# Optimization experiments

Hardware: AMD Instinct MI355X
Metric: run time of the kernel (lower is better)

Reference implementation:

```python
import jax, jax.numpy as jnp
import numpy as np

INPUT_SIZE = 500
SENTENCE_SIZE = 128


def setup_inputs() -> dict:
    key = jax.random.key(0)
    ks = jax.random.split(key, 20)
    B, D = 16, 512
    Ho, Hi, Hu = 4, 4, 4
    dh_ori = D // Ho          # 128
    dh = D // (Hi + Hu)       # 64
    s = 0.05
    code = jax.random.normal(ks[0], (B, INPUT_SIZE, D), jnp.float32)
    # binary sentence-membership mask (which code tokens belong to each sentence)
    input_sentence = (jax.random.uniform(ks[1], (B, SENTENCE_SIZE, INPUT_SIZE)) < 0.2).astype(jnp.float32)

    def W(k, h, dout):
        return jax.random.normal(k, (h, D, dout), jnp.float32) * s

    def b(k, h, dout):
        return jax.random.normal(k, (h, dout), jnp.float32) * 0.01

    return dict(
        code=code, input_sentence=input_sentence,
        Wq_ori=W(ks[2], Ho, dh_ori), bq_ori=b(ks[3], Ho, dh_ori),
        Wk_ori=W(ks[4], Ho, dh_ori), bk_ori=b(ks[5], Ho, dh_ori),
        Wq_in=W(ks[6], Hi, dh), bq_in=b(ks[7], Hi, dh),
        Wk_in=W(ks[8], Hi, dh), bk_in=b(ks[9], Hi, dh),
        Wv_in=W(ks[10], Hi, dh), bv_in=b(ks[11], Hi, dh),
        Wq_out=W(ks[12], Hu, dh), bq_out=b(ks[13], Hu, dh),
        Wk_out=W(ks[14], Hu, dh), bk_out=b(ks[15], Hu, dh),
        Wv_out=W(ks[16], Hu, dh), bv_out=b(ks[17], Hu, dh),
    )


def _proj(x, W, b):
    # x: (B, N, D), W: (H, D, F), b: (H, F) -> (B, H, N, F), relu Dense per head
    return jax.nn.relu(jnp.einsum('bnd,hdf->bhnf', x, W) + b[:, None, :])


def reference(code, input_sentence,
              Wq_ori, bq_ori, Wk_ori, bk_ori,
              Wq_in, bq_in, Wk_in, bk_in, Wv_in, bv_in,
              Wq_out, bq_out, Wk_out, bk_out, Wv_out, bv_out):
    B, S = input_sentence.shape[0], input_sentence.shape[1]
    sent = input_sentence

    # ---- original (ori) branch: max over heads of raw QK^T, mask, matmul code ----
    q = _proj(code, Wq_ori, bq_ori)
    k = _proj(code, Wk_ori, bk_ori)
    scores_ori = jnp.einsum('bhnf,bhmf->bhnm', q, k).max(axis=1)      # (B, N, N)
    sA = jnp.einsum('bsn,bnm->bsm', sent, scores_ori)                 # (B, S, N)
    out_ori = jnp.einsum('bsm,bmd->bsd', sent * sA, code)             # (B, S, D)

    # ---- in-mask heads ----
    qi = _proj(code, Wq_in, bq_in)
    ki = _proj(code, Wk_in, bk_in)
    vi = _proj(code, Wv_in, bv_in)
    sc = jnp.einsum('bhnf,bhmf->bhnm', qi, ki)                        # (B, Hi, N, N)
    sAi = jnp.einsum('bsn,bhnm->bhsm', sent, sc)                      # (B, Hi, S, N)
    out_in = jnp.einsum('bhsm,bhmf->bhsf', sent[:, None] * sAi, vi)   # (B, Hi, S, F)

    # ---- out-mask heads ----
    qo = _proj(code, Wq_out, bq_out)
    ko = _proj(code, Wk_out, bk_out)
    vo = _proj(code, Wv_out, bv_out)
    sco = jnp.einsum('bhnf,bhmf->bhnm', qo, ko)
    sAo = jnp.einsum('bsn,bhnm->bhsm', sent, sco)
    masked = (sent - 1.0)[:, None] * sAo                              # (B, Hu, S, N)
    include = sent.sum(axis=2)[:, None, :, None]                      # (B, 1, S, 1)
    masked = masked / (INPUT_SIZE - include) * include
    out_out = jnp.einsum('bhsm,bhmf->bhsf', masked, vo)               # (B, Hu, S, F)

    # original returns a list [ori, in_0..in_Hi-1, out_0..out_Hu-1]; concat along features
    in_flat = jnp.transpose(out_in, (0, 2, 1, 3)).reshape(B, S, -1)
    out_flat = jnp.transpose(out_out, (0, 2, 1, 3)).reshape(B, S, -1)
    return jnp.concatenate([out_ori, in_flat, out_flat], axis=-1)
```

## Files before the change

### kernel.cpp

```cpp
#include <hip/hip_runtime.h>
#include <cfloat>

#define B_  16
#define N_  500
#define NP  512
#define S_  128
#define D_  512
#define FO  128
#define FI  64

typedef unsigned short u16;
typedef __attribute__((ext_vector_type(8))) short bf8;
typedef __attribute__((ext_vector_type(4))) float f4;

#define MFMA(a,b,c) __builtin_amdgcn_mfma_f32_16x16x32_bf16((a),(b),(c),0,0,0)

__device__ __forceinline__ u16 f2b(float x){
    union{float f;unsigned u;} v; v.f=x;
    unsigned r = v.u + 0x7fffu + ((v.u>>16)&1u);
    return (u16)(r>>16);
}
__device__ __forceinline__ float b2f(u16 x){
    union{unsigned u;float f;} v; v.u=((unsigned)x)<<16; return v.f;
}
__device__ __forceinline__ bf8 ldb8(const u16* p){ return *(const bf8*)p; }

__device__ __forceinline__ void gl2lds16(const u16* g, u16* lds){
    __builtin_amdgcn_global_load_lds(
        (const __attribute__((address_space(1))) unsigned int*)g,
        (__attribute__((address_space(3))) unsigned int*)lds, 16, 0, 0);
}
__device__ __forceinline__ void vdrain(){
    asm volatile("s_waitcnt vmcnt(0)" ::: "memory");
}

struct PWAll { const float* W[8]; u16* WT[8]; };
__global__ __launch_bounds__(256) void prep_fused(const float* __restrict__ code,
                                                  u16* __restrict__ codeB,
                                                  u16* __restrict__ codeT,
                                                  PWAll a,
                                                  const float* __restrict__ sent,
                                                  u16* __restrict__ sentB,
                                                  float* __restrict__ inc,
                                                  u16* a0, u16* a1, u16* a2, u16* a3)
{
    __shared__ float T[64][65];
    const int t = threadIdx.x;
    const int x = blockIdx.x;
    if (x < 1024){
        const int b  = x >> 6;
        const int m0 = ((x >> 3) & 7) * 64;
        const int d0 = (x & 7) * 64;
        #pragma unroll
        for (int i=0;i<16;++i){
            int idx = t + i*256; int rr = idx>>6, cc = idx&63;
            int m = m0+rr;
            T[rr][cc] = (m < N_) ? code[((size_t)b*N_+m)*D_ + d0+cc] : 0.f;
        }
        __syncthreads();
        #pragma unroll
        for (int i=0;i<16;++i){
            int idx=t+i*256; int rr=idx>>6, cc=idx&63; int m=m0+rr;
            if (m<N_) codeB[((size_t)b*N_+m)*D_ + d0+cc] = f2b(T[rr][cc]);
        }
        #pragma unroll
        for (int i=0;i<16;++i){
            int idx=t+i*256; int dd=idx>>6, mm=idx&63;
            codeT[((size_t)b*D_ + d0+dd)*NP + m0+mm] = f2b(T[mm][dd]);
        }
    } else if (x < 1344){
        const int v    = x - 1024;
        const int h    = v / 80;
        const int rem  = v - h*80;
        const int slot = rem >> 3;
        const int d0   = (rem & 7) * 64;
        const int widx = slot<4 ? (slot>>1) : slot-2;
        const int ftile= slot<4 ? (slot&1)  : 0;
        const int F    = slot<4 ? 128 : 64;
        const float* W = a.W[widx];
        u16* WT        = a.WT[widx];
        const int f0 = ftile*64;
        #pragma unroll
        for (int i=0;i<16;++i){
            int idx=t+i*256; int rr=idx>>6, cc=idx&63;
            T[rr][cc] = W[((size_t)h*D_ + d0+rr)*F + f0+cc];
        }
        __syncthreads();
        #pragma unroll
        for (int i=0;i<16;++i){
            int idx=t+i*256; int ff=idx>>6, dd=idx&63;
            WT[((size_t)h*F + f0+ff)*D_ + d0+dd] = f2b(T[dd][ff]);
        }
    } else if (x < 2368){
        const int y  = x - 1344;
        const int b  = y >> 6;
        const int s  = (y & 63)*2 + (t >> 7);
        const int tl = t & 127;
        const float* row = sent + ((size_t)b*S_+s)*N_;
        float4 v = make_float4(0.f,0.f,0.f,0.f);
        const int n = tl*4;
        if (n < N_) v = *(const float4*)(row+n);
        float sum = v.x+v.y+v.z+v.w;
        ushort4 o; o.x=f2b(v.x); o.y=f2b(v.y); o.z=f2b(v.z); o.w=f2b(v.w);
        *(ushort4*)&sentB[((size_t)b*S_+s)*NP + n] = o;
        #pragma unroll
        for (int off=32; off; off>>=1) sum += __shfl_down(sum, off);
        __shared__ float ls[4];
        if ((t&63)==0) ls[t>>6]=sum;
        __syncthreads();
        if (tl==0) inc[b*S_+s] = ls[(t>>7)*2] + ls[(t>>7)*2+1];
    } else {
        const int u  = x - 2368;
        u16* arr4[4] = {a0,a1,a2,a3};
        u16* base = arr4[u>>6] + (size_t)(u&63)*FI*NP;
        for (int idx=t; idx<FI*12; idx+=256){
            int f = idx/12, n = N_ + idx%12;
            base[(size_t)f*NP + n] = 0;
        }
    }
}

struct GemmOut { const float* bias[8]; u16* dst[8]; };
union ProjLDS {
    u16 ab[4][4096];
    u16 ot[16896];
};
__global__ __launch_bounds__(256) void proj_gemm(const u16* __restrict__ codeB,
                                                 const u16* __restrict__ WallT,
                                                 GemmOut go)
{
    __shared__ alignas(16) ProjLDS L;

    const int t = threadIdx.x;
    const int w = t>>6, l = t&63, lane16 = l&15, lq = l>>4;
    const int bid = blockIdx.x;
    const int xcd = bid & 7;
    const int g   = bid >> 3;
    const int rt  = xcd*8 + g/20;
    const int ct  = g - (g/20)*20;
    const int r0 = rt*128;
    const int c0 = ct*128;
    const int wr = (w>>1)*64, wc = (w&1)*64;
    const int srow = l>>2;

    f4 acc[4][4] = {};

    auto STAGE = [&](u16* Ad, u16* Bd, int k0){
        #pragma unroll
        for (int iss=0; iss<2; ++iss){
            const int rbase = w*32 + iss*16;
            const int R  = rbase + srow;
            const int cg = ((l&3) ^ ((R>>1)&3))*8;
            gl2lds16(codeB + (size_t)(r0+R)*D_ + k0 + cg, Ad + rbase*32);
            gl2lds16(WallT + (size_t)(c0+R)*D_ + k0 + cg, Bd + rbase*32);
        }
    };
    auto COMPUTE = [&](const u16* Ad, const u16* Bd){
        bf8 af[4], bfr[4];
        #pragma unroll
        for (int i=0;i<4;++i){
            const int Ra = wr + i*16 + lane16;
            const int Rb = wc + i*16 + lane16;
            af[i]  = *(const bf8*)&Ad[Ra*32 + ((lq ^ ((Ra>>1)&3))*8)];
            bfr[i] = *(const bf8*)&Bd[Rb*32 + ((lq ^ ((Rb>>1)&3))*8)];
        }
        #pragma unroll
        for (int i=0;i<4;++i)
            #pragma unroll
            for (int j=0;j<4;++j)
                acc[i][j] = MFMA(af[i], bfr[j], acc[i][j]);
    };

    STAGE(L.ab[0], L.ab[2], 0);
    #pragma unroll
    for (int k0=0; k0<D_; k0+=64){
        vdrain(); __syncthreads();
        if (k0+32 < D_) STAGE(L.ab[1], L.ab[3], k0+32);
        COMPUTE(L.ab[0], L.ab[2]);
        vdrain(); __syncthreads();
        if (k0+64 < D_) STAGE(L.ab[0], L.ab[2], k0+64);
        COMPUTE(L.ab[1], L.ab[3]);
    }

    const int ri = (ct<4) ? 0 : (ct<8) ? 1 : 2 + ((ct-8)>>1);
    const bool tr = (ri==2)||(ri==4)||(ri==5)||(ri==7);

    vdrain(); __syncthreads();

    #pragma unroll
    for (int j=0;j<4;++j){
        const int c = c0 + wc + j*16 + lane16;
        const int idx = (c < 1024) ? (c & 511) : ((c-1024) & 255);
        const float bv = go.bias[ri][idx];
        if (tr){
            #pragma unroll
            for (int i=0;i<4;++i){
                ushort4 o4;
                float x0=acc[i][j][0]+bv, x1=acc[i][j][1]+bv, x2=acc[i][j][2]+bv, x3=acc[i][j][3]+bv;
                o4.x=f2b(x0>0.f?x0:0.f); o4.y=f2b(x1>0.f?x1:0.f);
                o4.z=f2b(x2>0.f?x2:0.f); o4.w=f2b(x3>0.f?x3:0.f);
                *(ushort4*)&L.ot[(wc+j*16+lane16)*132 + wr+i*16+lq*4] = o4;
            }
        } else {
            #pragma unroll
            for (int i=0;i<4;++i)
                #pragma unroll
                for (int reg=0;reg<4;++reg){
                    float x = acc[i][j][reg] + bv;
                    L.ot[(wr+i*16+lq*4+reg)*132 + wc+j*16+lane16] = f2b(x>0.f?x:0.f);
                }
        }
    }
    __syncthreads();

    if (tr){
        const int c  = t>>1;
        const int cg = c0 + c;
        const int u  = cg - 1024;
        const int hfv = u & 255, h = hfv>>6, f2 = hfv & 63;
        u16* dbase = go.dst[ri];
        const int half = t & 1;
        #pragma unroll
        for (int k2=0;k2<16;++k2){
            const int r  = half*64 + k2*4;
            const int rb = r0 + r;
            if (rb < 8000){
                const int b = rb/500, n = rb - b*500;
                *(ushort4*)&dbase[((size_t)(b*4+h)*FI + f2)*NP + n] =
                    *(const ushort4*)&L.ot[c*132 + r];
            }
        }
    } else {
        const int r  = t>>1;
        const int rb = r0 + r;
        if (rb < 8000){
            const int b = rb/500, n = rb - b*500;
            const int half = t & 1;
            const int cg0 = c0 + half*64;
            int h, f2base, F2;
            if (cg0 < 1024){ const int hf0 = cg0 & 511; h = hf0>>7; f2base = hf0 & 127; F2 = 128; }
            else           { const int hf0 = (cg0-1024) & 255; h = hf0>>6; f2base = hf0 & 63; F2 = 64; }
            u16* dstp = go.dst[ri] + ((size_t)(b*4+h)*N_ + n)*F2 + f2base;
            #pragma unroll
            for (int k2=0;k2<16;++k2)
                *(ushort4*)&dstp[k2*4] = *(const ushort4*)&L.ot[r*132 + half*64 + k2*4];
        }
    }
}

struct AttnArgs { const u16* qT[2]; const u16* kp[2]; const u16* vT[2]; };
struct MsLDS  { u16 Qs[64][136]; u16 Ks[128][136]; };
struct AtLDS  { float red[4][32][68]; u16 qsS[32][72]; u16 Pw[4][32][72]; };
union MALDS   { MsLDS ms; AtLDS at; };

__global__ __launch_bounds__(256) void msattn(const u16* __restrict__ q,
                                              const u16* __restrict__ k,
                                              u16* __restrict__ maxscT,
                                              AttnArgs a,
                                              const u16* __restrict__ sentB,
                                              const float* __restrict__ inc,
                                              float* __restrict__ out)
{
    __shared__ alignas(16) MALDS L;
    const int t=threadIdx.x, w=t>>6, l=t&63, lane16=l&15, lq=l>>4;
    const int idx = blockIdx.x >> 1;

    if ((blockIdx.x & 1) == 0){
        const int b=idx&15, n0=((idx>>4)&7)*64, m0=(idx>>7)*128;
        const int wr=(w>>1)*32, wc=(w&1)*64;

        f4 best[2][4];
        #pragma unroll
        for(int rt=0;rt<2;++rt)
            #pragma unroll
            for(int ct=0;ct<4;++ct)
                #pragma unroll
                for(int i=0;i<4;++i) best[rt][ct][i] = -FLT_MAX;

        for (int h=0;h<4;++h){
            const u16* qh = q + (size_t)(b*4+h)*N_*FO;
            const u16* kh = k + (size_t)(b*4+h)*N_*FO;
            #pragma unroll
            for (int i=0;i<4;++i){
                const int e=t+i*256, row=e>>4, kc=(e&15)*8;
                int n=n0+row; if(n>N_-1)n=N_-1;
                *(bf8*)&L.ms.Qs[row][kc] = ldb8(qh + (size_t)n*FO + kc);
            }
            #pragma unroll
            for (int i=0;i<8;++i){
                const int e=t+i*256, row=e>>4, kc=(e&15)*8;
                int m=m0+row; if(m>N_-1)m=N_-1;
                *(bf8*)&L.ms.Ks[row][kc] = ldb8(kh + (size_t)m*FO + kc);
            }
            __syncthreads();
            f4 acc[2][4]={};
            #pragma unroll
            for (int kk=0;kk<FO;kk+=32){
                bf8 a0=*(const bf8*)&L.ms.Qs[wr+lane16][kk+lq*8];
                bf8 a1=*(const bf8*)&L.ms.Qs[wr+16+lane16][kk+lq*8];
                #pragma unroll
                for(int ct=0;ct<4;++ct){
                    bf8 bb=*(const bf8*)&L.ms.Ks[wc+ct*16+lane16][kk+lq*8];
                    acc[0][ct]=MFMA(a0,bb,acc[0][ct]);
                    acc[1][ct]=MFMA(a1,bb,acc[1][ct]);
                }
            }
            #pragma unroll
            for(int rt=0;rt<2;++rt)
                #pragma unroll
                for(int ct=0;ct<4;++ct)
                    #pragma unroll
                    for(int i=0;i<4;++i) best[rt][ct][i] = fmaxf(best[rt][ct][i], acc[rt][ct][i]);
            __syncthreads();
        }
        #pragma unroll
        for(int rt=0;rt<2;++rt)
            #pragma unroll
            for(int ct=0;ct<4;++ct){
                const int m  = m0+wc+ct*16+lane16;
                const int nb = n0+wr+rt*16+lq*4;
                ushort4 o; o.x=f2b(best[rt][ct][0]); o.y=f2b(best[rt][ct][1]);
                o.z=f2b(best[rt][ct][2]); o.w=f2b(best[rt][ct][3]);
                *(ushort4*)&maxscT[((size_t)b*NP+m)*NP + nb] = o;
            }
    } else {
        const int bh=idx&63, b=bh>>2, h=bh&3, s0=((idx>>6)&3)*32, br=idx>>8;
        const u16* qT = a.qT[br];
        const u16* kp = a.kp[br];
        const u16* vT = a.vT[br];

        {
            const u16 *ap[2], *bp[4];
            #pragma unroll
            for(int rt=0;rt<2;++rt) ap[rt] = sentB + ((size_t)b*S_ + s0+rt*16+lane16)*NP + w*128 + lq*8;
            #pragma unroll
            for(int ct=0;ct<4;++ct) bp[ct] = qT + ((size_t)bh*FI + ct*16+lane16)*NP + w*128 + lq*8;
            f4 acc[2][4] = {};
            #pragma unroll
            for (int k0=0;k0<128;k0+=32){
                bf8 a0=ldb8(ap[0]+k0), a1=ldb8(ap[1]+k0);
                #pragma unroll
                for(int ct=0;ct<4;++ct){
                    bf8 bb=ldb8(bp[ct]+k0);
                    acc[0][ct]=MFMA(a0,bb,acc[0][ct]);
                    acc[1][ct]=MFMA(a1,bb,acc[1][ct]);
                }
            }
            #pragma unroll
            for(int rt=0;rt<2;++rt)
                #pragma unroll
                for(int ct=0;ct<4;++ct)
                    #pragma unroll
                    for(int reg=0;reg<4;++reg)
                        L.at.red[w][rt*16+lq*4+reg][ct*16+lane16] = acc[rt][ct][reg];
        }
        __syncthreads();
        {
            const int s=t>>3, f0=(t&7)*8;
            #pragma unroll
            for (int j=0;j<8;++j){
                float v = L.at.red[0][s][f0+j]+L.at.red[1][s][f0+j]
                        + L.at.red[2][s][f0+j]+L.at.red[3][s][f0+j];
                L.at.qsS[s][f0+j] = f2b(v);
            }
        }
        __syncthreads();

        f4 accO[2][4] = {};
        #pragma unroll
        for (int c=0;c<2;++c){
            const int m0 = w*64 + c*256;
            f4 p[2][4] = {};
            const u16* bp[4];
            #pragma unroll
            for(int ct=0;ct<4;++ct){
                int m=m0+ct*16+lane16; if(m>N_-1)m=N_-1;
                bp[ct] = kp + ((size_t)bh*N_+m)*FI + lq*8;
            }
            #pragma unroll
            for (int kk=0; kk<FI; kk+=32){
                bf8 a0 = *(const bf8*)&L.at.qsS[lane16][kk+lq*8];
                bf8 a1 = *(const bf8*)&L.at.qsS[16+lane16][kk+lq*8];
                #pragma unroll
                for(int ct=0;ct<4;++ct){
                    bf8 bb=ldb8(bp[ct]+kk);
                    p[0][ct]=MFMA(a0,bb,p[0][ct]);
                    p[1][ct]=MFMA(a1,bb,p[1][ct]);
                }
            }
            #pragma unroll
            for(int rt=0;rt<2;++rt)
                #pragma unroll
                for(int ct=0;ct<4;++ct){
                    const int m = m0+ct*16+lane16;
                    #pragma unroll
                    for(int reg=0;reg<4;++reg){
                        const int s = s0+rt*16+lq*4+reg;
                        const float sv = b2f(sentB[((size_t)b*S_+s)*NP+m]);
                        const float wgt = br ? ((m<N_)? sv-1.f : 0.f) : sv;
                        L.at.Pw[w][rt*16+lq*4+reg][ct*16+lane16] = f2b(p[rt][ct][reg]*wgt);
                    }
                }
            #pragma unroll
            for (int kk2=0; kk2<64; kk2+=32){
                bf8 a2[2];
                #pragma unroll
                for(int rt=0;rt<2;++rt) a2[rt] = *(const bf8*)&L.at.Pw[w][rt*16+lane16][kk2+lq*8];
                #pragma unroll
                for(int ct=0;ct<4;++ct){
                    bf8 vv = ldb8(vT + ((size_t)bh*FI + ct*16+lane16)*NP + m0+kk2+lq*8);
                    accO[0][ct]=MFMA(a2[0],vv,accO[0][ct]);
                    accO[1][ct]=MFMA(a2[1],vv,accO[1][ct]);
                }
            }
        }
        #pragma unroll
        for(int rt=0;rt<2;++rt)
            #pragma unroll
            for(int ct=0;ct<4;++ct)
                #pragma unroll
                for(int reg=0;reg<4;++reg)
                    L.at.red[w][rt*16+lq*4+reg][ct*16+lane16] = accO[rt][ct][reg];
        __syncthreads();
        {
            const int s=t>>3, f0=(t&7)*8;
            float fac = 1.f;
            if (br){ const float ic = inc[b*S_+s0+s]; fac = ic/(500.f-ic); }
            const size_t o = ((size_t)b*S_+s0+s)*1024 + (br?768:512) + h*FI + f0;
            #pragma unroll
            for (int j=0;j<8;++j){
                float v = L.at.red[0][s][f0+j]+L.at.red[1][s][f0+j]
                        + L.at.red[2][s][f0+j]+L.at.red[3][s][f0+j];
                out[o+j] = v*fac;
            }
        }
    }
}

__global__ __launch_bounds__(512) void saoo(const u16* __restrict__ sentB,
                                            const u16* __restrict__ maxscT,
                                            const u16* __restrict__ codeT,
                                            float* __restrict__ out)
{
    __shared__ u16 sAmS[16][520];
    const int b=blockIdx.x, s0=blockIdx.y*16;
    const int t=threadIdx.x, w=t>>6, l=t&63, lane16=l&15, lq=l>>4;

    {
        const int m0 = w*64;
        const u16* ap = sentB + ((size_t)b*S_ + s0+lane16)*NP + lq*8;
        const u16* bp[4];
        #pragma unroll
        for(int ct=0;ct<4;++ct) bp[ct] = maxscT + ((size_t)b*NP + m0+ct*16+lane16)*NP + lq*8;
        f4 acc[4] = {};
        for (int k0=0;k0<NP;k0+=32){
            bf8 av=ldb8(ap+k0);
            #pragma unroll
            for(int ct=0;ct<4;++ct) acc[ct]=MFMA(av, ldb8(bp[ct]+k0), acc[ct]);
        }
        #pragma unroll
        for(int ct=0;ct<4;++ct){
            const int m = m0+ct*16+lane16;
            #pragma unroll
            for(int reg=0;reg<4;++reg){
                const int s = s0+lq*4+reg;
                const float sv = b2f(sentB[((size_t)b*S_+s)*NP+m]);
                sAmS[lq*4+reg][m] = (sv != 0.f) ? f2b(acc[ct][reg]*sv) : (u16)0;
            }
        }
    }
    __syncthreads();
    {
        const int d0 = w*64;
        const u16* bp[4];
        #pragma unroll
        for(int ct=0;ct<4;++ct) bp[ct] = codeT + ((size_t)b*D_ + d0+ct*16+lane16)*NP + lq*8;
        f4 acc[4] = {};
        for (int k0=0;k0<NP;k0+=32){
            bf8 av = *(const bf8*)&sAmS[lane16][k0+lq*8];
            #pragma unroll
            for(int ct=0;ct<4;++ct) acc[ct]=MFMA(av, ldb8(bp[ct]+k0), acc[ct]);
        }
        #pragma unroll
        for(int ct=0;ct<4;++ct){
            const int d = d0+ct*16+lane16;
            #pragma unroll
            for(int reg=0;reg<4;++reg){
                const int s = s0+lq*4+reg;
                out[((size_t)b*S_+s)*1024 + d] = acc[ct][reg];
            }
        }
    }
}

extern "C" void kernel_launch(void* const* d_in, const int* in_sizes, int n_in,
                              void* d_out, int out_size, void* d_ws, size_t ws_size,
                              hipStream_t stream)
{
    const float* code   = (const float*)d_in[0];
    const float* sent   = (const float*)d_in[1];
    const float* Wq_ori = (const float*)d_in[2];
    const float* bq_ori = (const float*)d_in[3];
    const float* Wk_ori = (const float*)d_in[4];
    const float* bk_ori = (const float*)d_in[5];
    const float* Wq_in  = (const float*)d_in[6];
    const float* bq_in  = (const float*)d_in[7];
    const float* Wk_in  = (const float*)d_in[8];
    const float* bk_in  = (const float*)d_in[9];
    const float* Wv_in  = (const float*)d_in[10];
    const float* bv_in  = (const float*)d_in[11];
    const float* Wq_out = (const float*)d_in[12];
    const float* bq_out = (const float*)d_in[13];
    const float* Wk_out = (const float*)d_in[14];
    const float* bk_out = (const float*)d_in[15];
    const float* Wv_out = (const float*)d_in[16];
    const float* bv_out = (const float*)d_in[17];
    float* out = (float*)d_out;

    char* w = (char*)d_ws;
    u16*   codeB  = (u16*)(w);
    u16*   WallT  = (u16*)(w + 8388608);
    u16*   WTqo   = WallT;
    u16*   WTko   = WallT +  262144;
    u16*   WTqi   = WallT +  524288;
    u16*   WTki   = WallT +  655360;
    u16*   WTvi   = WallT +  786432;
    u16*   WTqu   = WallT +  917504;
    u16*   WTku   = WallT + 1048576;
    u16*   WTvu   = WallT + 1179648;
    u16*   sentB  = (u16*)(w + 11010048);
    float* incp   = (float*)(w + 13107200);
    u16* q_ori  = (u16*)(w + 13115392);
    u16* k_ori  = (u16*)(w + 21307392);
    u16* maxscT = (u16*)(w + 29499392);
    u16* codeT  = (u16*)(w + 37888000);
    u16* k_in   = (u16*)(w + 46276608);
    u16* k_out  = (u16*)(w + 50372608);
    u16* qT_in  = (u16*)(w + 54468608);
    u16* qT_out = (u16*)(w + 58662912);
    u16* vT_in  = (u16*)(w + 62857216);
    u16* vT_out = (u16*)(w + 67051520);

    PWAll pw;
    pw.W[0]=Wq_ori; pw.W[1]=Wk_ori; pw.W[2]=Wq_in; pw.W[3]=Wk_in;
    pw.W[4]=Wv_in;  pw.W[5]=Wq_out; pw.W[6]=Wk_out; pw.W[7]=Wv_out;
    pw.WT[0]=WTqo; pw.WT[1]=WTko; pw.WT[2]=WTqi; pw.WT[3]=WTki;
    pw.WT[4]=WTvi; pw.WT[5]=WTqu; pw.WT[6]=WTku; pw.WT[7]=WTvu;
    prep_fused<<<dim3(2624), 256, 0, stream>>>(code, codeB, codeT, pw,
                                               sent, sentB, incp,
                                               qT_in, qT_out, vT_in, vT_out);

    GemmOut go;
    go.bias[0]=bq_ori; go.bias[1]=bk_ori; go.bias[2]=bq_in; go.bias[3]=bk_in;
    go.bias[4]=bv_in;  go.bias[5]=bq_out; go.bias[6]=bk_out; go.bias[7]=bv_out;
    go.dst[0]=q_ori; go.dst[1]=k_ori; go.dst[2]=qT_in; go.dst[3]=k_in;
    go.dst[4]=vT_in; go.dst[5]=qT_out; go.dst[6]=k_out; go.dst[7]=vT_out;
    proj_gemm<<<dim3(1280), 256, 0, stream>>>(codeB, WallT, go);

    AttnArgs aa;
    aa.qT[0]=qT_in;  aa.qT[1]=qT_out;
    aa.kp[0]=k_in;   aa.kp[1]=k_out;
    aa.vT[0]=vT_in;  aa.vT[1]=vT_out;
    msattn<<<dim3(1024), 256, 0, stream>>>(q_ori, k_ori, maxscT, aa, sentB, incp, out);

    saoo<<<dim3(16,8), 512, 0, stream>>>(sentB, maxscT, codeT, out);
}
```

Measured before the change: 128.8 us.

## Triple-buffer projection GEMM K-loop with partial vmcnt waits and setprio

```diff
diff --git a/kernel.cpp b/kernel.cpp
--- a/kernel.cpp
+++ b/kernel.cpp
@@ -29,9 +29,6 @@
     __builtin_amdgcn_global_load_lds(
         (const __attribute__((address_space(1))) unsigned int*)g,
         (__attribute__((address_space(3))) unsigned int*)lds, 16, 0, 0);
-}
-__device__ __forceinline__ void vdrain(){
-    asm volatile("s_waitcnt vmcnt(0)" ::: "memory");
 }
 
 struct PWAll { const float* W[8]; u16* WT[8]; };
@@ -122,9 +119,46 @@
 
 struct GemmOut { const float* bias[8]; u16* dst[8]; };
 union ProjLDS {
-    u16 ab[4][4096];
+    u16 ab[6][4096];
     u16 ot[16896];
 };
+
+#define PG_WAIT(NN) asm volatile("s_waitcnt vmcnt(" #NN ")" ::: "memory")
+#define PG_FENCE()  asm volatile("" ::: "memory")
+
+#define PG_STAGE(ai, bi, kk) { \
+    gl2lds16(codeB + (size_t)(r0 + w*32      + srow)*D_ + (kk) + cgs, &L.ab[ai][(w*32)*32]);     \
+    gl2lds16(WallT + (size_t)(c0 + w*32      + srow)*D_ + (kk) + cgs, &L.ab[bi][(w*32)*32]);     \
+    gl2lds16(codeB + (size_t)(r0 + w*32 + 16 + srow)*D_ + (kk) + cgs, &L.ab[ai][(w*32+16)*32]);  \
+    gl2lds16(WallT + (size_t)(c0 + w*32 + 16 + srow)*D_ + (kk) + cgs, &L.ab[bi][(w*32+16)*32]);  \
+}
+
+#define PG_COMPUTE(ai, bi) { \
+    bf8 af[4], bfr[4]; \
+    _Pragma("unroll") \
+    for (int i=0;i<4;++i){ \
+        af[i]  = *(const bf8*)&L.ab[ai][(wr + i*16 + lane16)*32 + kread]; \
+        bfr[i] = *(const bf8*)&L.ab[bi][(wc + i*16 + lane16)*32 + kread]; \
+    } \
+    _Pragma("unroll") \
+    for (int i=0;i<4;++i) \
+        _Pragma("unroll") \
+        for (int j=0;j<4;++j) \
+            acc[i][j] = MFMA(af[i], bfr[j], acc[i][j]); \
+}
+
+#define PG_STEP(WN, ai, bi, jn) { \
+    PG_WAIT(WN); \
+    __builtin_amdgcn_s_barrier(); \
+    PG_FENCE(); \
+    __builtin_amdgcn_s_setprio(1); \
+    PG_COMPUTE(ai, bi); \
+    __builtin_amdgcn_s_setprio(0); \
+    __builtin_amdgcn_s_barrier(); \
+    PG_FENCE(); \
+    if ((jn) < 16) PG_STAGE(ai, bi, (jn)*32); \
+}
+
 __global__ __launch_bounds__(256) void proj_gemm(const u16* __restrict__ codeB,
                                                  const u16* __restrict__ WallT,
                                                  GemmOut go)
@@ -142,50 +176,36 @@
     const int c0 = ct*128;
     const int wr = (w>>1)*64, wc = (w&1)*64;
     const int srow = l>>2;
+    const int cgs  = ((l&3) ^ ((srow>>1)&3))*8;
+    const int kread= (lq ^ ((lane16>>1)&3))*8;
 
     f4 acc[4][4] = {};
 
-    auto STAGE = [&](u16* Ad, u16* Bd, int k0){
-        #pragma unroll
-        for (int iss=0; iss<2; ++iss){
-            const int rbase = w*32 + iss*16;
-            const int R  = rbase + srow;
-            const int cg = ((l&3) ^ ((R>>1)&3))*8;
-            gl2lds16(codeB + (size_t)(r0+R)*D_ + k0 + cg, Ad + rbase*32);
-            gl2lds16(WallT + (size_t)(c0+R)*D_ + k0 + cg, Bd + rbase*32);
-        }
-    };
-    auto COMPUTE = [&](const u16* Ad, const u16* Bd){
-        bf8 af[4], bfr[4];
-        #pragma unroll
-        for (int i=0;i<4;++i){
-            const int Ra = wr + i*16 + lane16;
-            const int Rb = wc + i*16 + lane16;
-            af[i]  = *(const bf8*)&Ad[Ra*32 + ((lq ^ ((Ra>>1)&3))*8)];
-            bfr[i] = *(const bf8*)&Bd[Rb*32 + ((lq ^ ((Rb>>1)&3))*8)];
-        }
-        #pragma unroll
-        for (int i=0;i<4;++i)
-            #pragma unroll
-            for (int j=0;j<4;++j)
-                acc[i][j] = MFMA(af[i], bfr[j], acc[i][j]);
-    };
-
-    STAGE(L.ab[0], L.ab[2], 0);
-    #pragma unroll
-    for (int k0=0; k0<D_; k0+=64){
-        vdrain(); __syncthreads();
-        if (k0+32 < D_) STAGE(L.ab[1], L.ab[3], k0+32);
-        COMPUTE(L.ab[0], L.ab[2]);
-        vdrain(); __syncthreads();
-        if (k0+64 < D_) STAGE(L.ab[0], L.ab[2], k0+64);
-        COMPUTE(L.ab[1], L.ab[3]);
-    }
+    PG_STAGE(0,3, 0);
+    PG_STAGE(1,4, 32);
+    PG_STAGE(2,5, 64);
+
+    PG_STEP(8, 0,3, 3);
+    PG_STEP(8, 1,4, 4);
+    PG_STEP(8, 2,5, 5);
+    PG_STEP(8, 0,3, 6);
+    PG_STEP(8, 1,4, 7);
+    PG_STEP(8, 2,5, 8);
+    PG_STEP(8, 0,3, 9);
+    PG_STEP(8, 1,4, 10);
+    PG_STEP(8, 2,5, 11);
+    PG_STEP(8, 0,3, 12);
+    PG_STEP(8, 1,4, 13);
+    PG_STEP(8, 2,5, 14);
+    PG_STEP(8, 0,3, 15);
+    PG_STEP(8, 1,4, 16);
+    PG_STEP(4, 2,5, 17);
+    PG_STEP(0, 0,3, 18);
 
     const int ri = (ct<4) ? 0 : (ct<8) ? 1 : 2 + ((ct-8)>>1);
     const bool tr = (ri==2)||(ri==4)||(ri==5)||(ri==7);
 
-    vdrain(); __syncthreads();
+    __syncthreads();
 
     #pragma unroll
     for (int j=0;j<4;++j){
```

After: 124.2 us, median of 2. -3.6%, faster.
